# Performance work log

Hardware: AMD Instinct MI355X
Metric: run time of the kernel (lower is better)

## Reference

```python
import jax, jax.numpy as jnp
import numpy as np

EPS = 1e-7
C_CONST = 1.0


def gru_scan(x_seq, h0, Wih, Whh, bih, bhh):
    # x_seq: [T,B,E], h0: [B,H]; torch GRU gate order: r, z, n
    xg = jnp.einsum('tbe,ge->tbg', x_seq, Wih) + bih  # [T,B,3H]

    def step(h, xg_t):
        hg = h @ Whh.T + bhh
        xr, xz, xn = jnp.split(xg_t, 3, axis=-1)
        hr, hz, hn = jnp.split(hg, 3, axis=-1)
        r = jax.nn.sigmoid(xr + hr)
        z = jax.nn.sigmoid(xz + hz)
        n = jnp.tanh(xn + r * hn)
        h_new = (1.0 - z) * n + z * h
        return h_new, h_new

    hT, outs = jax.lax.scan(step, h0, xg)
    return outs, hT


def e2lorentz(x):
    # Euclidean -> Lorentz: [..., D] -> [..., D+1]
    rr = jnp.linalg.norm(x, axis=-1, keepdims=True)
    unit = x / rr
    return jnp.concatenate([unit * jnp.sinh(rr), jnp.cosh(rr)], axis=-1)


def arcosh(x):
    return jnp.log(x) + jnp.log1p(jnp.sqrt(x * x - 1.0 + EPS) / x)


def setup_inputs() -> dict:
    key = jax.random.key(0)
    ks = jax.random.split(key, 14)
    T, B, E, H, V = 64, 1024, 300, 256, 50000
    s = 0.05
    inp = {}
    inp['tokens'] = jax.random.randint(ks[0], (T, B), 0, V, dtype=jnp.int32)
    inp['hidden_state'] = jnp.zeros((2, B, H), jnp.float32)
    inp['emb'] = jax.random.normal(ks[1], (V, E), jnp.float32) * s
    inp['Wih_f'] = jax.random.normal(ks[2], (3 * H, E), jnp.float32) * s
    inp['Whh_f'] = jax.random.normal(ks[3], (3 * H, H), jnp.float32) * s
    inp['bih_f'] = jax.random.normal(ks[4], (3 * H,), jnp.float32) * s
    inp['bhh_f'] = jax.random.normal(ks[5], (3 * H,), jnp.float32) * s
    inp['Wih_b'] = jax.random.normal(ks[6], (3 * H, E), jnp.float32) * s
    inp['Whh_b'] = jax.random.normal(ks[7], (3 * H, H), jnp.float32) * s
    inp['bih_b'] = jax.random.normal(ks[8], (3 * H,), jnp.float32) * s
    inp['bhh_b'] = jax.random.normal(ks[9], (3 * H,), jnp.float32) * s
    inp['attn_W'] = jax.random.normal(ks[10], (2 * H, 2 * H), jnp.float32) * s
    inp['attn_b'] = jax.random.normal(ks[11], (2 * H,), jnp.float32) * s
    inp['centroid'] = jax.random.normal(ks[12], (2 * H,), jnp.float32) * s
    inp['beta'] = jax.random.normal(ks[13], (1,), jnp.float32) * s
    return inp


def reference(tokens, hidden_state, emb, Wih_f, Whh_f, bih_f, bhh_f,
              Wih_b, Whh_b, bih_b, bhh_b, attn_W, attn_b, centroid, beta):
    x = emb[tokens]  # [T,B,E]
    f_fwd, h_f = gru_scan(x, hidden_state[0], Wih_f, Whh_f, bih_f, bhh_f)
    f_bwd_rev, h_b = gru_scan(x[::-1], hidden_state[1], Wih_b, Whh_b, bih_b, bhh_b)
    f_bwd = f_bwd_rev[::-1]
    f_output = jnp.concatenate([f_fwd, f_bwd], axis=-1)  # [T,B,2H]
    h_output = jnp.stack([h_f, h_b], axis=0)             # [2,B,H]

    # hyperbolic attention scores
    a = jnp.tanh(jnp.einsum('tbd,od->tbo', f_output, attn_W) + attn_b)
    aL = e2lorentz(a)                      # [T,B,2H+1]
    uL = e2lorentz(centroid[None, None, :])  # [1,1,2H+1]
    m = aL * uL
    prod = jnp.clip(-jnp.sum(m[..., :-1], axis=-1) + m[..., -1], 1.0 + EPS, 1e16)
    dist = arcosh(prod)                    # [T,B]
    score = -beta[0] * dist - C_CONST
    score = score - score.max()
    alpha = jax.nn.softmax(score, axis=0)  # softmax over time

    # Klein-model features with Lorentz-factor (gamma) weighted midpoint
    fL = e2lorentz(f_output)
    fK = fL[..., :-1] / jnp.clip(fL[..., -1:], EPS, 1e16)  # [T,B,2H]
    dump = jnp.sqrt(jnp.clip(1.0 - jnp.sum(fK * fK, axis=-1), EPS, 1.0 - EPS))
    gamma = jnp.clip(1.0 / dump, 1.0 + EPS, 1e16)
    alpha = alpha * gamma
    alpha = alpha / jnp.sum(alpha, axis=0)
    out = jnp.sum(alpha[..., None] * fK, axis=0)[None]  # [1,B,2H]
    return out, h_output
```

## Files before the change

### kernel.cpp

```cpp
#include <hip/hip_runtime.h>
#include <hip/hip_bf16.h>
#include <math.h>

#define T_  64
#define B_  1024
#define E_  300
#define EP_ 320
#define H_  256
#define G3_ 768
#define D_  512
#define CH_ 16

typedef float f32x4 __attribute__((ext_vector_type(4)));
typedef short bf16x8 __attribute__((ext_vector_type(8)));
typedef unsigned short u16x4 __attribute__((ext_vector_type(4)));

__device__ __forceinline__ float bf2f(unsigned short u){ return __uint_as_float(((unsigned)u) << 16); }
__device__ __forceinline__ unsigned short f2bf(float x){
    __hip_bfloat16 h = __float2bfloat16(x);
    return *(unsigned short*)&h;
}
__device__ __forceinline__ float fsig(float x){ return 1.0f/(1.0f + __expf(-x)); }
__device__ __forceinline__ float ftanh(float x){ return 2.0f/(1.0f + __expf(-2.0f*x)) - 1.0f; }

__global__ void lorentz_u_kernel(const float* __restrict__ centroid,
                                 float* __restrict__ su)
{
    __shared__ float red[512];
    const int tid = threadIdx.x;
    float c = centroid[tid];
    red[tid] = c*c;
    __syncthreads();
    for (int s = 256; s > 0; s >>= 1){
        if (tid < s) red[tid] += red[tid + s];
        __syncthreads();
    }
    float rr = sqrtf(red[0]);
    su[tid] = c / rr * sinhf(rr);
    if (tid == 0) su[512] = coshf(rr);
}

__global__ void cast_pad_kernel(const float* __restrict__ src,
                                __hip_bfloat16* __restrict__ dst,
                                int ncols, int ncols_pad)
{
    long long r = blockIdx.x;
    int c = threadIdx.x;
    float v = (c < ncols) ? src[r*ncols + c] : 0.f;
    dst[r*ncols_pad + c] = __float2bfloat16(v);
}

__global__ void prep_bias_kernel(const float* __restrict__ bihf, const float* __restrict__ bhhf,
                                 const float* __restrict__ bihb, const float* __restrict__ bhhb,
                                 float* __restrict__ biasc)
{
    int c = threadIdx.x, d = blockIdx.x;
    const float* bih = d ? bihb : bihf;
    const float* bhh = d ? bhhb : bhhf;
    biasc[d*G3_ + c] = bih[c] + (c < 2*H_ ? bhh[c] : 0.f);
}

__global__ __launch_bounds__(256) void proj_kernel(
    const int* __restrict__ tokens, int tlo_f, int tlo_b,
    const __hip_bfloat16* __restrict__ embbf,
    const __hip_bfloat16* __restrict__ wihf, const __hip_bfloat16* __restrict__ wihb,
    const float* __restrict__ biasc,
    __hip_bfloat16* __restrict__ xgf, __hip_bfloat16* __restrict__ xgb)
{
    __shared__ char As[64 * 640];
    __shared__ char Ws[64 * 640];
    const int dir = blockIdx.z;
    const int tlo = dir ? tlo_b : tlo_f;
    const __hip_bfloat16* Wbf = dir ? wihb : wihf;
    const float* bias = biasc + dir*G3_;
    __hip_bfloat16* xg = dir ? xgb : xgf;
    const int* tok = tokens + (long long)tlo * B_;

    const int tid = threadIdx.x;
    const int n0 = blockIdx.x * 64;

    {
        #pragma unroll
        for (int it = 0; it < 10; ++it){
            int idx = it*256 + tid;
            int col = idx / 40, u = idx - col*40;
            float4 v = *(const float4*)(Wbf + (size_t)(n0 + col)*EP_ + u*8);
            *(float4*)(Ws + col*640 + ((u ^ (col & 7)) * 16)) = v;
        }
    }

    const int lane = tid & 63, w = tid >> 6;
    const int g = lane >> 4, l15 = lane & 15;
    const int arow = w*16 + l15;
    const char* abase = As + arow * 640;
    const int amask = arow & 7;

    for (int rt = 0; rt < 4; ++rt){
        const int m0 = (blockIdx.y*4 + rt) * 64;
        {
            int row = tid >> 2, sub = tid & 3;
            long long tk = tok[m0 + row];
            const char* src = (const char*)(embbf + tk * EP_);
            char* dst = As + row * 640;
            int xm = (row & 7);
            #pragma unroll
            for (int j = 0; j < 10; ++j){
                int slot = sub + j*4;
                float4 v = *(const float4*)(src + slot*16);
                *(float4*)(dst + ((slot ^ xm) * 16)) = v;
            }
        }
        __syncthreads();

        f32x4 acc[4];
        #pragma unroll
        for (int i = 0; i < 4; ++i) acc[i] = (f32x4){0.f,0.f,0.f,0.f};

        #pragma unroll
        for (int kc = 0; kc < 10; ++kc){
            int aslot = kc*4 + g;
            bf16x8 a = *(const bf16x8*)(abase + ((aslot ^ amask) * 16));
            #pragma unroll
            for (int ct = 0; ct < 4; ++ct){
                int cl = ct*16 + l15;
                bf16x8 b = *(const bf16x8*)(Ws + cl*640 + ((aslot ^ (cl & 7)) * 16));
                acc[ct] = __builtin_amdgcn_mfma_f32_16x16x32_bf16(a, b, acc[ct], 0, 0, 0);
            }
        }

        #pragma unroll
        for (int ct = 0; ct < 4; ++ct){
            int col = n0 + ct*16 + l15;
            float bv = bias[col];
            int rbase = m0 + w*16 + g*4;
            #pragma unroll
            for (int i = 0; i < 4; ++i)
                xg[(long long)(rbase + i)*G3_ + col] = __float2bfloat16(acc[ct][i] + bv);
        }
        __syncthreads();
    }
}

__global__ __launch_bounds__(512, 1) void gru_chunk_kernel(
    const __hip_bfloat16* __restrict__ xg_f, const __hip_bfloat16* __restrict__ xg_b,
    int tlo_f, int tlo_b,
    __hip_bfloat16* __restrict__ f_bf,
    float* __restrict__ hf32g,
    const float* __restrict__ hidden,
    const __hip_bfloat16* __restrict__ whhbf,
    const float* __restrict__ bhh_f, const float* __restrict__ bhh_b,
    float* __restrict__ hout, int s0)
{
    __shared__ char hlds[2][16 * 512];
    __shared__ char xlds[2][16 * 1536];
    __shared__ float blds[256];
    const int bid = blockIdx.x;
    const int dir = bid & 1;
    const int b0 = (bid >> 1) * 16;
    const int tid = threadIdx.x;
    const int lane = tid & 63, w = tid >> 6;
    const int g = lane >> 4, l15 = lane & 15;
    const int jq = w*32 + g*4;

    const __hip_bfloat16* xg = dir ? xg_b : xg_f;
    const int tlo = dir ? tlo_b : tlo_f;
    const float* bhh = dir ? bhh_b : bhh_f;
    const __hip_bfloat16* Wb = whhbf + (size_t)dir * G3_ * H_;
    float* hfg = hf32g + (size_t)dir * B_ * H_;
    const int b = b0 + l15;

    bf16x8 Wf[3][2][8];
    #pragma unroll
    for (int gate = 0; gate < 3; ++gate)
        #pragma unroll
        for (int tl = 0; tl < 2; ++tl)
            #pragma unroll
            for (int kc = 0; kc < 8; ++kc)
                Wf[gate][tl][kc] = *(const bf16x8*)(Wb +
                    ((size_t)(gate*H_ + w*32 + tl*16 + l15))*H_ + kc*32 + g*8);

    if (tid < 256) blds[tid] = bhh[2*H_ + tid];

    const float* hsrc = (s0 == 0 ? hidden : hf32g) + (size_t)dir * B_ * H_;
    #pragma unroll
    for (int it = 0; it < 2; ++it){
        int idx = it*512 + tid;
        int r = idx >> 6, q = idx & 63;
        float4 v = *(const float4*)(hsrc + ((size_t)(b0 + r))*H_ + q*4);
        unsigned short t4[4] = { f2bf(v.x), f2bf(v.y), f2bf(v.z), f2bf(v.w) };
        *(uint2*)(hlds[0] + r*512 + (((q>>1) ^ (r&7))*16) + (q&1)*8) = *(uint2*)t4;
    }
    f32x4 carry[2];
    #pragma unroll
    for (int tl = 0; tl < 2; ++tl)
        carry[tl] = *(const f32x4*)&hsrc[(size_t)b*H_ + jq + tl*16];

    auto stage_x = [&](char* dst, const __hip_bfloat16* xgt){
        #pragma unroll
        for (int i = 0; i < 3; ++i){
            int U = (i*8 + w)*64 + lane;
            int r = U / 96;
            int sbase = U - r*96;
            int usrc = sbase - r; if (usrc < 0) usrc += 96;
            const char* src = (const char*)xgt + (size_t)(b0 + r)*1536 + usrc*16;
            __builtin_amdgcn_global_load_lds(
                (const __attribute__((address_space(1))) void*)src,
                (__attribute__((address_space(3))) void*)(dst + (i*8 + w)*1024),
                16, 0, 0);
        }
    };
    {
        const int t0 = dir ? (63 - s0) : s0;
        stage_x(xlds[0], xg + (size_t)(t0 - tlo)*B_*G3_);
    }
    __syncthreads();

    int cur = 0, hc = 0;
    u16x4 pend[2];
    int t_pend = -1;
    for (int s = s0; s < s0 + CH_; ++s){
        const int t = dir ? (63 - s) : s;

        if (s < s0 + CH_ - 1){
            const int tn = dir ? (t - 1) : (t + 1);
            stage_x(xlds[cur ^ 1], xg + (size_t)(tn - tlo)*B_*G3_);
        }

        f32x4 acc[3][2];
        #pragma unroll
        for (int gate = 0; gate < 3; ++gate)
            #pragma unroll
            for (int tl = 0; tl < 2; ++tl)
                acc[gate][tl] = (f32x4){0.f,0.f,0.f,0.f};

        {
            bf16x8 hb[4];
            #pragma unroll
            for (int kc = 0; kc < 4; ++kc)
                hb[kc] = *(const bf16x8*)(hlds[hc] + l15*512 + (((kc*4 + g) ^ (l15&7))*16));
            #pragma unroll
            for (int kc = 0; kc < 4; ++kc)
                #pragma unroll
                for (int gate = 0; gate < 3; ++gate)
                    #pragma unroll
                    for (int tl = 0; tl < 2; ++tl)
                        acc[gate][tl] = __builtin_amdgcn_mfma_f32_16x16x32_bf16(
                            Wf[gate][tl][kc], hb[kc], acc[gate][tl], 0, 0, 0);
        }
        {
            bf16x8 hb[4];
            #pragma unroll
            for (int kc = 0; kc < 4; ++kc)
                hb[kc] = *(const bf16x8*)(hlds[hc] + l15*512 + ((((kc+4)*4 + g) ^ (l15&7))*16));
            #pragma unroll
            for (int kc = 0; kc < 4; ++kc)
                #pragma unroll
                for (int gate = 0; gate < 3; ++gate)
                    #pragma unroll
                    for (int tl = 0; tl < 2; ++tl)
                        acc[gate][tl] = __builtin_amdgcn_mfma_f32_16x16x32_bf16(
                            Wf[gate][tl][kc+4], hb[kc], acc[gate][tl], 0, 0, 0);
        }

        u16x4 outv[2];
        #pragma unroll
        for (int tl = 0; tl < 2; ++tl){
            u16x4 xv[3];
            #pragma unroll
            for (int gate = 0; gate < 3; ++gate){
                int u = gate*32 + w*4 + tl*2 + (g >> 1);
                int sl = u + l15; if (sl >= 96) sl -= 96;
                xv[gate] = *(const u16x4*)(xlds[cur] + l15*1536 + sl*16 + (g & 1)*8);
            }
            f32x4 bhn = *(const f32x4*)&blds[jq + tl*16];

            unsigned short hb4[4];
            float hn4[4];
            #pragma unroll
            for (int i = 0; i < 4; ++i){
                float xr = bf2f(xv[0][i]);
                float xz = bf2f(xv[1][i]);
                float xn = bf2f(xv[2][i]);
                float r_ = fsig(xr + acc[0][tl][i]);
                float z_ = fsig(xz + acc[1][tl][i]);
                float n_ = ftanh(xn + r_*(acc[2][tl][i] + bhn[i]));
                float hnew = (1.f - z_)*n_ + z_*carry[tl][i];
                carry[tl][i] = hnew;
                hn4[i] = hnew;
                hb4[i] = f2bf(hnew);
            }
            int j0 = jq + tl*16;
            int slot = j0 >> 3;
            *(uint2*)(hlds[hc^1] + l15*512 + ((slot ^ (l15&7))*16) + (j0&7)*2) = *(uint2*)hb4;
            outv[tl] = *(u16x4*)hb4;
            if (s == 63)
                *(float4*)&hout[(size_t)dir*B_*H_ + (size_t)b*H_ + j0] = *(float4*)hn4;
        }

        if (s & 1){
            if (t_pend >= 0){
                #pragma unroll
                for (int tl = 0; tl < 2; ++tl)
                    *(u16x4*)((char*)f_bf + (((size_t)t_pend*B_ + b)*D_ + dir*H_ + jq + tl*16)*2) = pend[tl];
            }
            #pragma unroll
            for (int tl = 0; tl < 2; ++tl)
                *(u16x4*)((char*)f_bf + (((size_t)t*B_ + b)*D_ + dir*H_ + jq + tl*16)*2) = outv[tl];
            t_pend = -1;
        } else {
            pend[0] = outv[0]; pend[1] = outv[1];
            t_pend = t;
        }

        __syncthreads();
        cur ^= 1; hc ^= 1;
    }

    #pragma unroll
    for (int tl = 0; tl < 2; ++tl)
        *(f32x4*)&hfg[(size_t)b*H_ + jq + tl*16] = carry[tl];
}

__global__ __launch_bounds__(256) void attn_score_kernel(
    const __hip_bfloat16* __restrict__ f_bf, const __hip_bfloat16* __restrict__ Wbf,
    const float* __restrict__ attn_b, const float* __restrict__ su,
    const float* __restrict__ beta, float* __restrict__ score,
    float* __restrict__ rr2)
{
    __shared__ char WL[2][32 * 1024];
    const int tid = threadIdx.x;
    const int lane = tid & 63, w = tid >> 6;
    const int g = lane >> 4, l15 = lane & 15;
    const long long m0 = (long long)blockIdx.x * 64;
    const long long arow = m0 + w*16 + l15;

    bf16x8 a[16];
    const __hip_bfloat16* ap = f_bf + arow*D_;
    #pragma unroll
    for (int kc = 0; kc < 16; ++kc)
        a[kc] = *(const bf16x8*)(ap + kc*32 + g*8);

    {
        float s2 = 0.f;
        #pragma unroll
        for (int kc = 0; kc < 16; ++kc){
            const unsigned short* hb = (const unsigned short*)&a[kc];
            #pragma unroll
            for (int q = 0; q < 8; ++q){ float x = bf2f(hb[q]); s2 += x*x; }
        }
        s2 += __shfl_xor(s2, 16);
        s2 += __shfl_xor(s2, 32);
        if (g == 0) rr2[arow] = s2;
    }

    auto stage_w = [&](char* dst, int nc){
        const __hip_bfloat16* wsrc = Wbf + (size_t)nc*32*D_;
        #pragma unroll
        for (int i = 0; i < 8; ++i){
            int U = i*256 + tid;
            int r = U >> 6, sl = U & 63;
            int usrc = (sl - r) & 63;
            const char* src = (const char*)(wsrc + (size_t)r*D_) + usrc*16;
            __builtin_amdgcn_global_load_lds(
                (const __attribute__((address_space(1))) void*)src,
                (__attribute__((address_space(3))) void*)(dst + U*16),
                16, 0, 0);
        }
    };

    stage_w(WL[0], 0);
    __syncthreads();

    float pdot[4] = {0,0,0,0}, pa2[4] = {0,0,0,0};
    int cur = 0;

    for (int nc = 0; nc < 16; ++nc){
        if (nc < 15) stage_w(WL[cur ^ 1], nc + 1);

        f32x4 acc[2];
        acc[0] = (f32x4){0.f,0.f,0.f,0.f};
        acc[1] = (f32x4){0.f,0.f,0.f,0.f};
        #pragma unroll
        for (int kc = 0; kc < 16; ++kc){
            int u = kc*4 + g;
            #pragma unroll
            for (int ct = 0; ct < 2; ++ct){
                int cl = ct*16 + l15;
                bf16x8 bfr = *(const bf16x8*)(WL[cur] + cl*1024 + (((u + cl) & 63)*16));
                acc[ct] = __builtin_amdgcn_mfma_f32_16x16x32_bf16(a[kc], bfr, acc[ct], 0, 0, 0);
            }
        }

        #pragma unroll
        for (int ct = 0; ct < 2; ++ct){
            int col = nc*32 + ct*16 + l15;
            float bc = attn_b[col], sc = su[col];
            #pragma unroll
            for (int i = 0; i < 4; ++i){
                float av = ftanh(acc[ct][i] + bc);
                pdot[i] += av*sc;
                pa2[i]  += av*av;
            }
        }

        __syncthreads();
        cur ^= 1;
    }

    #pragma unroll
    for (int m = 1; m < 16; m <<= 1){
        #pragma unroll
        for (int i = 0; i < 4; ++i){
            pdot[i] += __shfl_xor(pdot[i], m);
            pa2[i]  += __shfl_xor(pa2[i],  m);
        }
    }
    if (l15 == 0){
        const float cu = su[512], bb = beta[0];
        #pragma unroll
        for (int i = 0; i < 4; ++i){
            long long row = m0 + w*16 + g*4 + i;
            float ra  = sqrtf(pa2[i]);
            float shc = sinhf(ra)/ra;
            float prod = cu*coshf(ra) - shc*pdot[i];
            prod = fminf(fmaxf(prod, 1.0f + 1e-7f), 1e16f);
            float dist = logf(prod) + log1pf(sqrtf(prod*prod - 1.0f + 1e-7f)/prod);
            score[row] = -bb * dist;
        }
    }
}

__global__ __launch_bounds__(256) void pool_kernel(
    const __hip_bfloat16* __restrict__ f_bf, const float* __restrict__ score,
    const float* __restrict__ rr2, float* __restrict__ out)
{
    __shared__ float wss[64];
    const int tid = threadIdx.x;
    const long long b = blockIdx.x;

    if (tid < 64){
        int t = tid;
        float sc = score[t*B_ + b];
        float mx = sc;
        #pragma unroll
        for (int m = 1; m < 64; m <<= 1) mx = fmaxf(mx, __shfl_xor(mx, m));
        float e = expf(sc - mx);
        float rr = sqrtf(rr2[t*B_ + b]);
        float th = tanhf(rr);
        float omt = 1.0f - th*th;
        omt = fminf(fmaxf(omt, 1e-7f), 1.0f - 1e-7f);
        float gamma = 1.0f / sqrtf(omt);
        gamma = fminf(fmaxf(gamma, 1.0f + 1e-7f), 1e16f);
        float wgt = e * gamma;
        float ssum = wgt;
        #pragma unroll
        for (int m = 1; m < 64; m <<= 1) ssum += __shfl_xor(ssum, m);
        wss[t] = (wgt / ssum) * (th / rr);
    }
    __syncthreads();

    #pragma unroll
    for (int dd = 0; dd < 2; ++dd){
        int d = tid + dd*256;
        float acc = 0.f;
        for (int t = 0; t < 64; ++t)
            acc += wss[t] * __bfloat162float(f_bf[((long long)t*B_ + b)*D_ + d]);
        out[b*D_ + d] = acc;
    }
}

extern "C" void kernel_launch(void* const* d_in, const int* in_sizes, int n_in,
                              void* d_out, int out_size, void* d_ws, size_t ws_size,
                              hipStream_t stream)
{
    const int*   tokens = (const int*)  d_in[0];
    const float* hidden = (const float*)d_in[1];
    const float* emb    = (const float*)d_in[2];
    const float* Wih_f  = (const float*)d_in[3];
    const float* Whh_f  = (const float*)d_in[4];
    const float* bih_f  = (const float*)d_in[5];
    const float* bhh_f  = (const float*)d_in[6];
    const float* Wih_b  = (const float*)d_in[7];
    const float* Whh_b  = (const float*)d_in[8];
    const float* bih_b  = (const float*)d_in[9];
    const float* bhh_b  = (const float*)d_in[10];
    const float* attn_W = (const float*)d_in[11];
    const float* attn_b = (const float*)d_in[12];
    const float* centroid = (const float*)d_in[13];
    const float* beta   = (const float*)d_in[14];

    const int V = in_sizes[2] / E_;

    char* w = (char*)d_ws;
    __hip_bfloat16* f_bf  = (__hip_bfloat16*)w;  w += (size_t)T_*B_*D_*2;
    __hip_bfloat16* xg_f  = (__hip_bfloat16*)w;  w += (size_t)CH_*B_*G3_*2;
    __hip_bfloat16* xg_b  = (__hip_bfloat16*)w;  w += (size_t)CH_*B_*G3_*2;
    float*          hf32g = (float*)w;           w += (size_t)2*B_*H_*4;
    __hip_bfloat16* embbf = (__hip_bfloat16*)w;  w += (size_t)V*EP_*2;
    __hip_bfloat16* wihf  = (__hip_bfloat16*)w;  w += (size_t)G3_*EP_*2;
    __hip_bfloat16* wihb  = (__hip_bfloat16*)w;  w += (size_t)G3_*EP_*2;
    __hip_bfloat16* whhbf = (__hip_bfloat16*)w;  w += (size_t)2*G3_*H_*2;
    __hip_bfloat16* wat   = (__hip_bfloat16*)w;  w += (size_t)D_*D_*2;
    float*          biasc = (float*)w;           w += (size_t)2*G3_*4;
    float*          score = (float*)w;           w += (size_t)T_*B_*4;
    float*          rr2   = (float*)w;           w += (size_t)T_*B_*4;
    float*          su    = (float*)w;           w += 513*4;

    float* out  = (float*)d_out;
    float* hout = out + (long long)B_*D_;

    lorentz_u_kernel<<<1, 512, 0, stream>>>(centroid, su);
    prep_bias_kernel<<<2, G3_, 0, stream>>>(bih_f, bhh_f, bih_b, bhh_b, biasc);
    cast_pad_kernel<<<V,   EP_, 0, stream>>>(emb,    embbf, E_, EP_);
    cast_pad_kernel<<<G3_, EP_, 0, stream>>>(Wih_f,  wihf,  E_, EP_);
    cast_pad_kernel<<<G3_, EP_, 0, stream>>>(Wih_b,  wihb,  E_, EP_);
    cast_pad_kernel<<<G3_, H_,  0, stream>>>(Whh_f,  whhbf,            H_, H_);
    cast_pad_kernel<<<G3_, H_,  0, stream>>>(Whh_b,  whhbf + (size_t)G3_*H_, H_, H_);
    cast_pad_kernel<<<D_,  D_,  0, stream>>>(attn_W, wat,   D_, D_);

    for (int c = 0; c < T_/CH_; ++c){
        int tlo_f = c*CH_;
        int tlo_b = (T_ - CH_) - c*CH_;
        int s0 = c*CH_;
        proj_kernel<<<dim3(12, 64, 2), 256, 0, stream>>>(
            tokens, tlo_f, tlo_b, embbf, wihf, wihb, biasc, xg_f, xg_b);
        gru_chunk_kernel<<<128, 512, 0, stream>>>(
            xg_f, xg_b, tlo_f, tlo_b, f_bf, hf32g, hidden,
            whhbf, bhh_f, bhh_b, hout, s0);
    }

    attn_score_kernel<<<1024, 256, 0, stream>>>(f_bf, wat, attn_b, su, beta, score, rr2);
    pool_kernel<<<1024, 256, 0, stream>>>(f_bf, score, rr2, out);
}
```

Baseline: 620.0 us.

## Prefetch embedding rows into registers and reorder GRU recurrence MFMA loop

In the input projection kernel, the embedding gather for the next row tile is now loaded into registers while the current tile's MFMAs run, double-buffering through register arrays instead of loading synchronously before each barrier. In the recurrent kernel, the hidden-state MFMA loop is restructured to load h fragments two at a time, interleaved with the MFMAs, and is wrapped in s_setprio to raise wave priority. The pairwise buffered write of f_bf outputs is replaced by direct per-step stores. The register prefetch adds register pressure, and the direct stores give up write batching.

```diff
diff --git a/kernel.cpp b/kernel.cpp
--- a/kernel.cpp
+++ b/kernel.cpp
@@ -78,6 +78,8 @@
 
     const int tid = threadIdx.x;
     const int n0 = blockIdx.x * 64;
+    const int row = tid >> 2, sub = tid & 3;
+    const int xm = row & 7;
 
     {
         #pragma unroll
@@ -95,22 +97,36 @@
     const char* abase = As + arow * 640;
     const int amask = arow & 7;
 
+    float4 avA[10], avB[10];
+    {
+        long long tk = tok[blockIdx.y*4*64 + row];
+        const char* src = (const char*)(embbf + tk * EP_);
+        #pragma unroll
+        for (int j = 0; j < 10; ++j)
+            avA[j] = *(const float4*)(src + (sub + j*4)*16);
+    }
+
+    #pragma unroll
     for (int rt = 0; rt < 4; ++rt){
         const int m0 = (blockIdx.y*4 + rt) * 64;
+        float4* avc = (rt & 1) ? avB : avA;
+        float4* avn = (rt & 1) ? avA : avB;
+
         {
-            int row = tid >> 2, sub = tid & 3;
-            long long tk = tok[m0 + row];
+            char* dst = As + row * 640;
+            #pragma unroll
+            for (int j = 0; j < 10; ++j)
+                *(float4*)(dst + (((sub + j*4) ^ xm) * 16)) = avc[j];
+        }
+        __syncthreads();
+
+        if (rt < 3){
+            long long tk = tok[m0 + 64 + row];
             const char* src = (const char*)(embbf + tk * EP_);
-            char* dst = As + row * 640;
-            int xm = (row & 7);
-            #pragma unroll
-            for (int j = 0; j < 10; ++j){
-                int slot = sub + j*4;
-                float4 v = *(const float4*)(src + slot*16);
-                *(float4*)(dst + ((slot ^ xm) * 16)) = v;
-            }
-        }
-        __syncthreads();
+            #pragma unroll
+            for (int j = 0; j < 10; ++j)
+                avn[j] = *(const float4*)(src + (sub + j*4)*16);
+        }
 
         f32x4 acc[4];
         #pragma unroll
@@ -216,8 +232,6 @@
     __syncthreads();
 
     int cur = 0, hc = 0;
-    u16x4 pend[2];
-    int t_pend = -1;
     for (int s = s0; s < s0 + CH_; ++s){
         const int t = dir ? (63 - s) : s;
 
@@ -233,36 +247,26 @@
             for (int tl = 0; tl < 2; ++tl)
                 acc[gate][tl] = (f32x4){0.f,0.f,0.f,0.f};
 
-        {
-            bf16x8 hb[4];
-            #pragma unroll
-            for (int kc = 0; kc < 4; ++kc)
-                hb[kc] = *(const bf16x8*)(hlds[hc] + l15*512 + (((kc*4 + g) ^ (l15&7))*16));
-            #pragma unroll
-            for (int kc = 0; kc < 4; ++kc)
+        __builtin_amdgcn_s_setprio(1);
+        #pragma unroll
+        for (int kh = 0; kh < 4; ++kh){
+            bf16x8 hb0 = *(const bf16x8*)(hlds[hc] + l15*512 + ((((2*kh  )*4 + g) ^ (l15&7))*16));
+            bf16x8 hb1 = *(const bf16x8*)(hlds[hc] + l15*512 + ((((2*kh+1)*4 + g) ^ (l15&7))*16));
+            #pragma unroll
+            for (int gate = 0; gate < 3; ++gate)
                 #pragma unroll
-                for (int gate = 0; gate < 3; ++gate)
-                    #pragma unroll
-                    for (int tl = 0; tl < 2; ++tl)
-                        acc[gate][tl] = __builtin_amdgcn_mfma_f32_16x16x32_bf16(
-                            Wf[gate][tl][kc], hb[kc], acc[gate][tl], 0, 0, 0);
-        }
-        {
-            bf16x8 hb[4];
-            #pragma unroll
-            for (int kc = 0; kc < 4; ++kc)
-                hb[kc] = *(const bf16x8*)(hlds[hc] + l15*512 + ((((kc+4)*4 + g) ^ (l15&7))*16));
-            #pragma unroll
-            for (int kc = 0; kc < 4; ++kc)
+                for (int tl = 0; tl < 2; ++tl)
+                    acc[gate][tl] = __builtin_amdgcn_mfma_f32_16x16x32_bf16(
+                        Wf[gate][tl][2*kh], hb0, acc[gate][tl], 0, 0, 0);
+            #pragma unroll
+            for (int gate = 0; gate < 3; ++gate)
                 #pragma unroll
-                for (int gate = 0; gate < 3; ++gate)
-                    #pragma unroll
-                    for (int tl = 0; tl < 2; ++tl)
-                        acc[gate][tl] = __builtin_amdgcn_mfma_f32_16x16x32_bf16(
-                            Wf[gate][tl][kc+4], hb[kc], acc[gate][tl], 0, 0, 0);
-        }
-
-        u16x4 outv[2];
+                for (int tl = 0; tl < 2; ++tl)
+                    acc[gate][tl] = __builtin_amdgcn_mfma_f32_16x16x32_bf16(
+                        Wf[gate][tl][2*kh+1], hb1, acc[gate][tl], 0, 0, 0);
+        }
+        __builtin_amdgcn_s_setprio(0);
+
         #pragma unroll
         for (int tl = 0; tl < 2; ++tl){
             u16x4 xv[3];
@@ -275,7 +279,6 @@
             f32x4 bhn = *(const f32x4*)&blds[jq + tl*16];
 
             unsigned short hb4[4];
-            float hn4[4];
             #pragma unroll
             for (int i = 0; i < 4; ++i){
                 float xr = bf2f(xv[0][i]);
@@ -286,30 +289,14 @@
                 float n_ = ftanh(xn + r_*(acc[2][tl][i] + bhn[i]));
                 float hnew = (1.f - z_)*n_ + z_*carry[tl][i];
                 carry[tl][i] = hnew;
-                hn4[i] = hnew;
                 hb4[i] = f2bf(hnew);
             }
             int j0 = jq + tl*16;
             int slot = j0 >> 3;
             *(uint2*)(hlds[hc^1] + l15*512 + ((slot ^ (l15&7))*16) + (j0&7)*2) = *(uint2*)hb4;
-            outv[tl] = *(u16x4*)hb4;
+            *(u16x4*)((char*)f_bf + (((size_t)t*B_ + b)*D_ + dir*H_ + j0)*2) = *(u16x4*)hb4;
             if (s == 63)
-                *(float4*)&hout[(size_t)dir*B_*H_ + (size_t)b*H_ + j0] = *(float4*)hn4;
-        }
-
-        if (s & 1){
-            if (t_pend >= 0){
-                #pragma unroll
-                for (int tl = 0; tl < 2; ++tl)
-                    *(u16x4*)((char*)f_bf + (((size_t)t_pend*B_ + b)*D_ + dir*H_ + jq + tl*16)*2) = pend[tl];
-            }
-            #pragma unroll
-            for (int tl = 0; tl < 2; ++tl)
-                *(u16x4*)((char*)f_bf + (((size_t)t*B_ + b)*D_ + dir*H_ + jq + tl*16)*2) = outv[tl];
-            t_pend = -1;
-        } else {
-            pend[0] = outv[0]; pend[1] = outv[1];
-            t_pend = t;
+                *(f32x4*)&hout[(size_t)dir*B_*H_ + (size_t)b*H_ + j0] = carry[tl];
         }
 
         __syncthreads();
```

After: 866.0 us. 1.4x slower.
